# Optimization experiments

Hardware: AMD Instinct MI355X
Metric: run time of the kernel (lower is better)

The kernel has to match this reference:

```python
import jax, jax.numpy as jnp
import numpy as np

B, IN_DIM, OUT_DIM, MV = 8192, 256, 256, 8


def setup_inputs() -> dict:
    key = jax.random.key(0)
    k1, k2 = jax.random.split(key)
    x = jax.random.normal(k1, (B, IN_DIM, MV), dtype=jnp.float32)
    weights = jax.random.normal(k2, (IN_DIM, OUT_DIM, MV), dtype=jnp.float32) * 0.01
    bias = jnp.zeros((OUT_DIM, MV), dtype=jnp.float32)
    return {"x": x, "weights": weights, "bias": bias}


def reference(x, weights, bias):
    # Simplified GA-3D geometric product, summed over in_dim (j), per out_dim (i):
    #   y[..., i, 0] = sum_j x[..., j, 0]*W[j,i,0] + x[..., j, 1]*W[j,i,1] + x[..., j, 2]*W[j,i,2]
    #   y[..., i, 4] = sum_j x[..., j, 1]*W[j,i,2] - x[..., j, 2]*W[j,i,1] + x[..., j, 4]*W[j,i,0]
    #   all other multivector components receive only the bias.
    # Scalar component: dot over first 3 multivector slots.
    c0 = jnp.einsum('bjk,jik->bi', x[..., 0:3], weights[..., 0:3])  # (B, OUT_DIM)
    # Bivector component e23: x1*w2 - x2*w1 + x4*w0.
    xv = jnp.stack([x[..., 1], -x[..., 2], x[..., 4]], axis=-1)          # (B, IN_DIM, 3)
    wv = jnp.stack([weights[..., 2], weights[..., 1], weights[..., 0]], axis=-1)  # (IN_DIM, OUT_DIM, 3)
    c4 = jnp.einsum('bjk,jik->bi', xv, wv)  # (B, OUT_DIM)
    y = jnp.broadcast_to(bias, (x.shape[0],) + bias.shape)  # (B, OUT_DIM, MV)
    y = y.at[..., 0].add(c0).at[..., 4].add(c4)
    return y
```

## Files before the change

### kernel.cpp

```cpp
#include <hip/hip_runtime.h>
#include <hip/hip_bf16.h>

typedef __attribute__((ext_vector_type(4))) float f32x4;
typedef __attribute__((ext_vector_type(8))) short bf16x8;
typedef __attribute__((ext_vector_type(4))) short short4v;

#define AROW 264
#define CS 516

__device__ __forceinline__ short f2bf(float f) {
  __hip_bfloat16 h = __float2bfloat16(f);
  return __builtin_bit_cast(short, h);
}

__global__ __launch_bounds__(256) void ga_prep_B(const float* __restrict__ W,
                                                 short* __restrict__ Bp) {
  const int gid = blockIdx.x * 256 + threadIdx.x;
  const int l  = gid & 63;
  const int cg = (gid >> 6) & 31;
  const int it = gid >> 11;
  const int ln = l & 15, q = l >> 4;
  const int hc = cg >> 4;
  const int i  = (cg & 15) * 16 + ln;
  const int j0 = it * 8 + q * 2;
  const float4* W4 = (const float4*)W;

  bf16x8 o;
#pragma unroll
  for (int jj = 0; jj < 2; ++jj) {
    const float4 wv = W4[((j0 + jj) * 256 + i) * 2];
    if (!hc) {
      o[jj * 4 + 0] = f2bf(wv.x); o[jj * 4 + 1] = f2bf(wv.y);
      o[jj * 4 + 2] = f2bf(wv.z); o[jj * 4 + 3] = 0;
    } else {
      o[jj * 4 + 0] = 0;           o[jj * 4 + 1] = f2bf(wv.z);
      o[jj * 4 + 2] = f2bf(-wv.y); o[jj * 4 + 3] = f2bf(wv.x);
    }
  }
  *(bf16x8*)&Bp[(size_t)gid * 8] = o;
}

__global__ __launch_bounds__(1024, 4) void ga_mv_main(
    const float* __restrict__ x, const short* __restrict__ Bp,
    const float* __restrict__ bias, float* __restrict__ y) {
  __shared__ __align__(16) char smem[33792];
  short* Abuf[2] = {(short*)smem, (short*)(smem + 32 * AROW * 2)};
  float* c_lds = (float*)smem;

  const int t = threadIdx.x;
  const int bm = blockIdx.x;
  const int lane = t & 63, w = t >> 6;
  const int ln = lane & 15, qq = lane >> 4;
  const int R0 = bm * 32;

  const int ci = t & 127, rb = t >> 7;
  const int jl = ci >> 1, h2 = ci & 1;
  const float4* x4 = (const float4*)x;
  float4 fr[4];

#define LOADX(qtr)                                                           \
  {                                                                          \
    _Pragma("unroll")                                                        \
    for (int i = 0; i < 4; ++i)                                              \
      fr[i] = x4[(size_t)(R0 + rb + 8 * i) * 512 + (qtr) * 128 + ci];        \
  }

#define PROC(dst)                                                            \
  {                                                                          \
    _Pragma("unroll")                                                        \
    for (int i = 0; i < 4; ++i) {                                            \
      const float c4 = __shfl_xor(fr[i].x, 1, 64);                           \
      if (!h2) {                                                             \
        short4v a;                                                           \
        a[0] = f2bf(fr[i].x); a[1] = f2bf(fr[i].y);                          \
        a[2] = f2bf(fr[i].z); a[3] = f2bf(c4);                               \
        *(short4v*)&(dst)[(rb + 8 * i) * AROW + jl * 4] = a;                 \
      }                                                                      \
    }                                                                        \
  }

  const size_t bbase = (size_t)w * 1024 + lane * 8;
  bf16x8 Bf[4][2];
#define LB(itv, b)                                                           \
  {                                                                          \
    const short* p = Bp + (size_t)(itv) * 16384 + bbase;                     \
    Bf[b][0] = *(const bf16x8*)(p);                                          \
    Bf[b][1] = *(const bf16x8*)(p + 512);                                    \
  }

  LOADX(0);
  PROC(Abuf[0]);
  __syncthreads();
  LB(0, 0);
  LB(1, 1);
  LB(2, 2);
  LB(3, 3);
  LOADX(1);

  f32x4 acc[2][2] = {};

#pragma unroll
  for (int q = 0; q < 4; ++q) {
    const short* Ac = Abuf[q & 1];
#pragma unroll
    for (int tau = 0; tau < 8; ++tau) {
      const int it = q * 8 + tau;
      if (tau == 4 && q < 3) {
        PROC(Abuf[(q + 1) & 1]);
        if (q < 2) LOADX(q + 2);
      }
      const bf16x8 af0 = *(const bf16x8*)&Ac[ln * AROW + (tau * 8 + qq * 2) * 4];
      const bf16x8 af1 = *(const bf16x8*)&Ac[(16 + ln) * AROW + (tau * 8 + qq * 2) * 4];
#pragma unroll
      for (int n = 0; n < 2; ++n) {
        acc[0][n] = __builtin_amdgcn_mfma_f32_16x16x32_bf16(af0, Bf[it & 3][n],
                                                            acc[0][n], 0, 0, 0);
        acc[1][n] = __builtin_amdgcn_mfma_f32_16x16x32_bf16(af1, Bf[it & 3][n],
                                                            acc[1][n], 0, 0, 0);
      }
      if (it + 4 < 32) LB(it + 4, it & 3);
    }
    __syncthreads();
  }

  const int h = t & 1, p = (t >> 1) & 255, rh = t >> 9;
  const float4 bv = ((const float4*)bias)[p * 2 + h];
  f32x4* y4 = (f32x4*)y;

#pragma unroll
  for (int ep = 0; ep < 2; ++ep) {
    if (ep) __syncthreads();
#pragma unroll
    for (int n = 0; n < 2; ++n)
#pragma unroll
      for (int r = 0; r < 4; ++r)
        c_lds[(qq * 4 + r) * CS + w * 32 + n * 16 + ln] = acc[ep][n][r];
    __syncthreads();
#pragma unroll
    for (int rr = 0; rr < 8; ++rr) {
      const int row = rr * 2 + rh;
      f32x4 o;
      o[0] = bv.x; o[1] = bv.y; o[2] = bv.z; o[3] = bv.w;
      o[0] += c_lds[row * CS + h * 256 + p];
      __builtin_nontemporal_store(
          o, &y4[((size_t)(R0 + ep * 16 + row) * 256 + p) * 2 + h]);
    }
  }
}

extern "C" void kernel_launch(void* const* d_in, const int* in_sizes, int n_in,
                              void* d_out, int out_size, void* d_ws, size_t ws_size,
                              hipStream_t stream) {
  const float* x = (const float*)d_in[0];
  const float* W = (const float*)d_in[1];
  const float* bias = (const float*)d_in[2];
  float* y = (float*)d_out;
  short* Bp = (short*)d_ws;

  ga_prep_B<<<dim3(256), dim3(256), 0, stream>>>(W, Bp);
  ga_mv_main<<<dim3(256), dim3(1024), 0, stream>>>(x, Bp, bias, y);
}
```

Measured before the change: 128.7 us.

## Pre-convert x to swizzled bf16 buffer and load it via global_load_lds

Adds a separate prep kernel that converts x to a packed bf16 A matrix with an XOR-swizzled layout. The main kernel then pulls its whole 32-row A tile straight into LDS with direct global-to-LDS loads, which removes the in-kernel fp32 load, shuffle and convert pipeline and the per-quarter barriers. In exchange it adds an extra kernel launch plus a write and re-read of a bf16 copy of x through global memory, and doubles LDS use per block.

```diff
diff --git a/kernel.cpp b/kernel.cpp
--- a/kernel.cpp
+++ b/kernel.cpp
@@ -3,15 +3,18 @@
 
 typedef __attribute__((ext_vector_type(4))) float f32x4;
 typedef __attribute__((ext_vector_type(8))) short bf16x8;
-typedef __attribute__((ext_vector_type(4))) short short4v;
 
-#define AROW 264
 #define CS 516
 
 __device__ __forceinline__ short f2bf(float f) {
   __hip_bfloat16 h = __float2bfloat16(f);
   return __builtin_bit_cast(short, h);
 }
+
+#define GLD_LDS16(gp, lp)                                                    \
+  __builtin_amdgcn_global_load_lds(                                          \
+      (const __attribute__((address_space(1))) unsigned int*)(gp),           \
+      (__attribute__((address_space(3))) unsigned int*)(lp), 16, 0, 0)
 
 __global__ __launch_bounds__(256) void ga_prep_B(const float* __restrict__ W,
                                                  short* __restrict__ Bp) {
@@ -40,44 +43,37 @@
   *(bf16x8*)&Bp[(size_t)gid * 8] = o;
 }
 
+__global__ __launch_bounds__(256) void ga_prep_A(const float* __restrict__ x,
+                                                 short* __restrict__ A) {
+  const int g = blockIdx.x * 256 + threadIdx.x;
+  const int row = g >> 7, rem = g & 127;
+  const int q = rem >> 5, c = rem & 31;
+  const int cp = c ^ ((row & 7) << 2);
+  const float4* x4 = (const float4*)x + (size_t)(row * 256 + q * 64 + c * 2) * 2;
+  const float4 a0 = x4[0], a1 = x4[1], b0 = x4[2], b1 = x4[3];
+  bf16x8 o;
+  o[0] = f2bf(a0.x); o[1] = f2bf(a0.y); o[2] = f2bf(a0.z); o[3] = f2bf(a1.x);
+  o[4] = f2bf(b0.x); o[5] = f2bf(b0.y); o[6] = f2bf(b0.z); o[7] = f2bf(b1.x);
+  *(bf16x8*)&A[((size_t)row * 128 + q * 32 + cp) * 8] = o;
+}
+
 __global__ __launch_bounds__(1024, 4) void ga_mv_main(
-    const float* __restrict__ x, const short* __restrict__ Bp,
+    const short* __restrict__ A, const short* __restrict__ Bp,
     const float* __restrict__ bias, float* __restrict__ y) {
-  __shared__ __align__(16) char smem[33792];
-  short* Abuf[2] = {(short*)smem, (short*)(smem + 32 * AROW * 2)};
+  __shared__ __align__(16) char smem[65536];
+  short* lds_s = (short*)smem;
   float* c_lds = (float*)smem;
 
   const int t = threadIdx.x;
   const int bm = blockIdx.x;
   const int lane = t & 63, w = t >> 6;
-  const int ln = lane & 15, qq = lane >> 4;
+  const int ln = lane & 15, qq = lane >> 4, lnl = lane & 7;
   const int R0 = bm * 32;
 
-  const int ci = t & 127, rb = t >> 7;
-  const int jl = ci >> 1, h2 = ci & 1;
-  const float4* x4 = (const float4*)x;
-  float4 fr[4];
-
-#define LOADX(qtr)                                                           \
-  {                                                                          \
-    _Pragma("unroll")                                                        \
-    for (int i = 0; i < 4; ++i)                                              \
-      fr[i] = x4[(size_t)(R0 + rb + 8 * i) * 512 + (qtr) * 128 + ci];        \
-  }
-
-#define PROC(dst)                                                            \
-  {                                                                          \
-    _Pragma("unroll")                                                        \
-    for (int i = 0; i < 4; ++i) {                                            \
-      const float c4 = __shfl_xor(fr[i].x, 1, 64);                           \
-      if (!h2) {                                                             \
-        short4v a;                                                           \
-        a[0] = f2bf(fr[i].x); a[1] = f2bf(fr[i].y);                          \
-        a[2] = f2bf(fr[i].z); a[3] = f2bf(c4);                               \
-        *(short4v*)&(dst)[(rb + 8 * i) * AROW + jl * 4] = a;                 \
-      }                                                                      \
-    }                                                                        \
-  }
+  const short* asrc = A + ((size_t)(R0 + (t >> 5)) * 128 + (t & 31)) * 8;
+#pragma unroll
+  for (int q = 0; q < 4; ++q)
+    GLD_LDS16(asrc + q * 256, lds_s + q * 8192 + t * 8);
 
   const size_t bbase = (size_t)w * 1024 + lane * 8;
   bf16x8 Bf[4][2];
@@ -87,41 +83,31 @@
     Bf[b][0] = *(const bf16x8*)(p);                                          \
     Bf[b][1] = *(const bf16x8*)(p + 512);                                    \
   }
-
-  LOADX(0);
-  PROC(Abuf[0]);
-  __syncthreads();
   LB(0, 0);
   LB(1, 1);
   LB(2, 2);
   LB(3, 3);
-  LOADX(1);
+
+  __syncthreads();
 
   f32x4 acc[2][2] = {};
-
+  const int abase = ln * 256 + qq * 8;
 #pragma unroll
-  for (int q = 0; q < 4; ++q) {
-    const short* Ac = Abuf[q & 1];
+  for (int it = 0; it < 32; ++it) {
+    const int q = it >> 3, tau = it & 7;
+    const short* Aq = lds_s + q * 8192 + abase + ((tau ^ lnl) << 5);
+    const bf16x8 af0 = *(const bf16x8*)Aq;
+    const bf16x8 af1 = *(const bf16x8*)(Aq + 4096);
 #pragma unroll
-    for (int tau = 0; tau < 8; ++tau) {
-      const int it = q * 8 + tau;
-      if (tau == 4 && q < 3) {
-        PROC(Abuf[(q + 1) & 1]);
-        if (q < 2) LOADX(q + 2);
-      }
-      const bf16x8 af0 = *(const bf16x8*)&Ac[ln * AROW + (tau * 8 + qq * 2) * 4];
-      const bf16x8 af1 = *(const bf16x8*)&Ac[(16 + ln) * AROW + (tau * 8 + qq * 2) * 4];
-#pragma unroll
-      for (int n = 0; n < 2; ++n) {
-        acc[0][n] = __builtin_amdgcn_mfma_f32_16x16x32_bf16(af0, Bf[it & 3][n],
-                                                            acc[0][n], 0, 0, 0);
-        acc[1][n] = __builtin_amdgcn_mfma_f32_16x16x32_bf16(af1, Bf[it & 3][n],
-                                                            acc[1][n], 0, 0, 0);
-      }
-      if (it + 4 < 32) LB(it + 4, it & 3);
+    for (int n = 0; n < 2; ++n) {
+      acc[0][n] = __builtin_amdgcn_mfma_f32_16x16x32_bf16(af0, Bf[it & 3][n],
+                                                          acc[0][n], 0, 0, 0);
+      acc[1][n] = __builtin_amdgcn_mfma_f32_16x16x32_bf16(af1, Bf[it & 3][n],
+                                                          acc[1][n], 0, 0, 0);
     }
-    __syncthreads();
+    if (it + 4 < 32) LB(it + 4, it & 3);
   }
+  __syncthreads();
 
   const int h = t & 1, p = (t >> 1) & 255, rh = t >> 9;
   const float4 bv = ((const float4*)bias)[p * 2 + h];
@@ -156,7 +142,9 @@
   const float* bias = (const float*)d_in[2];
   float* y = (float*)d_out;
   short* Bp = (short*)d_ws;
+  short* A = (short*)d_ws + (1 << 19);
 
   ga_prep_B<<<dim3(256), dim3(256), 0, stream>>>(W, Bp);
-  ga_mv_main<<<dim3(256), dim3(1024), 0, stream>>>(x, Bp, bias, y);
+  ga_prep_A<<<dim3(4096), dim3(256), 0, stream>>>(x, A);
+  ga_mv_main<<<dim3(256), dim3(1024), 0, stream>>>(A, Bp, bias, y);
 }
```

Measured after the change: 133.4 us. 1.04x slower.
